# Performance work log

Hardware: AMD Instinct MI355X
Metric: run time of the kernel (lower is better)

The kernel has to match this reference:

```python
import jax, jax.numpy as jnp
import numpy as np
from jax import lax


def _gauss1d(size, sigma):
    k = np.arange(size, dtype=np.float32) - (size - 1) / 2.0
    k = np.exp(-0.5 * (k / sigma) ** 2)
    return k / k.sum()


def _make_kernel(scale, sigma):
    # make_odd
    kx, ky, kz = [s + 1 if s % 2 == 0 else s for s in scale]
    kH = _gauss1d(kx, sigma)
    kW = _gauss1d(ky, sigma)
    kD = _gauss1d(kz, sigma)
    kern = kH[:, None, None] * kW[None, :, None] * kD[None, None, :]  # (kx, ky, kz)
    kern = np.transpose(kern, (2, 0, 1))  # permute(2,0,1) -> (kz, kx, ky)
    return jnp.asarray(kern, dtype=jnp.float32)


def setup_inputs() -> dict:
    key = jax.random.key(0)
    x = jax.random.normal(key, (2, 1, 256, 256, 256), dtype=jnp.float32)
    kernel0 = _make_kernel((2, 2, 2), 1.0)  # (3,3,3)
    kernel1 = _make_kernel((4, 4, 4), 1.0)  # (5,5,5)
    return {"x": x, "kernel0": kernel0, "kernel1": kernel1}


def _blur_down(x, kernel, stride):
    # replicate pad by k//2 per spatial dim, then depthwise (C=1) conv3d.
    pad = [(0, 0), (0, 0)] + [(k // 2, k // 2) for k in kernel.shape]
    xp = jnp.pad(x, pad, mode='edge')
    # strided VALID conv == full blur followed by [::s] slicing (output ceil(H/s))
    return lax.conv_general_dilated(
        xp, kernel[None, None].astype(x.dtype),
        window_strides=stride, padding='VALID',
        dimension_numbers=('NCDHW', 'OIDHW', 'NCDHW'))


def reference(x, kernel0, kernel1):
    d1 = _blur_down(x, kernel0, (2, 2, 2))  # (2,1,128,128,128)
    d2 = _blur_down(x, kernel1, (4, 4, 4))  # (2,1,64,64,64)
    return (x, d1, d2)
```

## Files before the change

### kernel.cpp

```cpp
#include <hip/hip_runtime.h>

#define N_BATCH 2
#define S_IN 256
#define S_D1 128
#define S_D2 64
#define IN_PER_BATCH (S_IN * S_IN * S_IN)
#define D1_PER_BATCH (S_D1 * S_D1 * S_D1)
#define D2_PER_BATCH (S_D2 * S_D2 * S_D2)
#define X_ELEMS (N_BATCH * IN_PER_BATCH)
#define D1_ELEMS (N_BATCH * D1_PER_BATCH)
#define D2_ELEMS (N_BATCH * D2_PER_BATCH)

__global__ __launch_bounds__(256) void d1_kernel(
    const float* __restrict__ x, const float* __restrict__ kern,
    float* __restrict__ out)
{
    __shared__ float kw[27];
    if (threadIdx.x < 27) kw[threadIdx.x] = kern[threadIdx.x];
    __syncthreads();

    int t = blockIdx.x * blockDim.x + threadIdx.x;
    if (t >= D1_ELEMS) return;

    int w = t & (S_D1 - 1);
    int h = (t >> 7) & (S_D1 - 1);
    int d = (t >> 14) & (S_D1 - 1);
    int n = t >> 21;

    const float* xb = x + (size_t)n * IN_PER_BATCH;

    float acc = 0.0f;
#pragma unroll
    for (int a = 0; a < 3; ++a) {
        int iz = 2 * d - 1 + a;
        iz = iz < 0 ? 0 : (iz > S_IN - 1 ? S_IN - 1 : iz);
#pragma unroll
        for (int b = 0; b < 3; ++b) {
            int iy = 2 * h - 1 + b;
            iy = iy < 0 ? 0 : (iy > S_IN - 1 ? S_IN - 1 : iy);
            const float* row = xb + ((size_t)iz * S_IN + iy) * S_IN;
            const float* kr = kw + (a * 3 + b) * 3;
#pragma unroll
            for (int c = 0; c < 3; ++c) {
                int ix = 2 * w - 1 + c;
                ix = ix < 0 ? 0 : (ix > S_IN - 1 ? S_IN - 1 : ix);
                acc = fmaf(kr[c], row[ix], acc);
            }
        }
    }
    out[t] = acc;
}

__global__ __launch_bounds__(256) void d2_kernel(
    const float* __restrict__ x, const float* __restrict__ kern,
    float* __restrict__ out)
{
    __shared__ float kw[125];
    if (threadIdx.x < 125) kw[threadIdx.x] = kern[threadIdx.x];
    __syncthreads();

    int t = blockIdx.x * blockDim.x + threadIdx.x;
    if (t >= D2_ELEMS) return;

    int w = t & (S_D2 - 1);
    int h = (t >> 6) & (S_D2 - 1);
    int d = (t >> 12) & (S_D2 - 1);
    int n = t >> 18;

    const float* xb = x + (size_t)n * IN_PER_BATCH;

    float acc = 0.0f;
#pragma unroll
    for (int a = 0; a < 5; ++a) {
        int iz = 4 * d - 2 + a;
        iz = iz < 0 ? 0 : (iz > S_IN - 1 ? S_IN - 1 : iz);
#pragma unroll
        for (int b = 0; b < 5; ++b) {
            int iy = 4 * h - 2 + b;
            iy = iy < 0 ? 0 : (iy > S_IN - 1 ? S_IN - 1 : iy);
            const float* row = xb + ((size_t)iz * S_IN + iy) * S_IN;
            const float* kr = kw + (a * 5 + b) * 5;
#pragma unroll
            for (int c = 0; c < 5; ++c) {
                int ix = 4 * w - 2 + c;
                ix = ix < 0 ? 0 : (ix > S_IN - 1 ? S_IN - 1 : ix);
                acc = fmaf(kr[c], row[ix], acc);
            }
        }
    }
    out[t] = acc;
}

extern "C" void kernel_launch(void* const* d_in, const int* in_sizes, int n_in,
                              void* d_out, int out_size, void* d_ws, size_t ws_size,
                              hipStream_t stream) {
    const float* x  = (const float*)d_in[0];
    const float* k0 = (const float*)d_in[1];
    const float* k1 = (const float*)d_in[2];

    float* out0 = (float*)d_out;
    float* out1 = out0 + X_ELEMS;
    float* out2 = out1 + D1_ELEMS;

    hipMemcpyAsync(out0, x, (size_t)X_ELEMS * sizeof(float),
                   hipMemcpyDeviceToDevice, stream);

    {
        int threads = 256;
        int blocks = (D1_ELEMS + threads - 1) / threads;
        d1_kernel<<<blocks, threads, 0, stream>>>(x, k0, out1);
    }

    {
        int threads = 256;
        int blocks = (D2_ELEMS + threads - 1) / threads;
        d2_kernel<<<blocks, threads, 0, stream>>>(x, k1, out2);
    }
}
```

Baseline: 318.4 us.

## Fuse identity copy and both blur-downsample levels into one LDS-tiled kernel

Replaces the device-to-device memcpy and the two separate strided-blur kernels with a single kernel. Each block loads a haloed 12x12x72 tile of the input into shared memory using float4 loads with edge clamping. From that tile it writes the identity copy, the 3x3x3 stride-2 output and the 5x5x5 stride-4 output, reducing the latter across 4 lanes with shuffles. The goal is to read the input once instead of three times and to remove the uncoalesced global gathers. The cost is halo over-fetch of about 2.5x per tile, which relies on L2 for neighbouring tiles, plus about 41KB of LDS per block.

```diff
diff --git a/kernel.cpp b/kernel.cpp
--- a/kernel.cpp
+++ b/kernel.cpp
@@ -1,94 +1,139 @@
 #include <hip/hip_runtime.h>
 
-#define N_BATCH 2
 #define S_IN 256
 #define S_D1 128
 #define S_D2 64
 #define IN_PER_BATCH (S_IN * S_IN * S_IN)
 #define D1_PER_BATCH (S_D1 * S_D1 * S_D1)
 #define D2_PER_BATCH (S_D2 * S_D2 * S_D2)
-#define X_ELEMS (N_BATCH * IN_PER_BATCH)
-#define D1_ELEMS (N_BATCH * D1_PER_BATCH)
-#define D2_ELEMS (N_BATCH * D2_PER_BATCH)
+#define X_ELEMS (2 * IN_PER_BATCH)
+#define D1_ELEMS (2 * D1_PER_BATCH)
+#define D2_ELEMS (2 * D2_PER_BATCH)
 
-__global__ __launch_bounds__(256) void d1_kernel(
-    const float* __restrict__ x, const float* __restrict__ kern,
-    float* __restrict__ out)
+#define TD 8
+#define TH 8
+#define TW 64
+#define LZ (TD + 4)
+#define LY (TH + 4)
+#define LX (TW + 8)
+#define LDS_ELEMS (LZ * LY * LX)
+
+__global__ __launch_bounds__(256) void fused_pyramid(
+    const float* __restrict__ x, const float* __restrict__ k0,
+    const float* __restrict__ k1, float* __restrict__ out0,
+    float* __restrict__ out1, float* __restrict__ out2)
 {
-    __shared__ float kw[27];
-    if (threadIdx.x < 27) kw[threadIdx.x] = kern[threadIdx.x];
-    __syncthreads();
+    __shared__ float ls[LDS_ELEMS];
+    __shared__ float kw0[27];
+    __shared__ float kw1[125];
 
-    int t = blockIdx.x * blockDim.x + threadIdx.x;
-    if (t >= D1_ELEMS) return;
+    const int tid = threadIdx.x;
+    if (tid < 27) kw0[tid] = k0[tid];
+    else if (tid >= 32 && tid < 32 + 125) kw1[tid - 32] = k1[tid - 32];
 
-    int w = t & (S_D1 - 1);
-    int h = (t >> 7) & (S_D1 - 1);
-    int d = (t >> 14) & (S_D1 - 1);
-    int n = t >> 21;
+    const int bx = blockIdx.x;
+    const int wt = bx & 3;
+    const int hy = (bx >> 2) & 31;
+    const int dz = (bx >> 7) & 31;
+    const int n  = bx >> 12;
+
+    const int x0 = wt * TW;
+    const int y0 = hy * TH;
+    const int z0 = dz * TD;
 
     const float* xb = x + (size_t)n * IN_PER_BATCH;
 
-    float acc = 0.0f;
+    for (int v = tid; v < 144 * 18; v += 256) {
+        int row = v / 18;
+        int j   = v - row * 18;
+        int lz  = row / LY;
+        int ly  = row - lz * LY;
+        int gz = z0 + lz - 2; gz = gz < 0 ? 0 : (gz > S_IN - 1 ? S_IN - 1 : gz);
+        int gy = y0 + ly - 2; gy = gy < 0 ? 0 : (gy > S_IN - 1 ? S_IN - 1 : gy);
+        const float* rp = xb + ((size_t)gz * S_IN + gy) * S_IN;
+        int gx = x0 - 4 + 4 * j;
+        float4 val;
+        if (gx >= 0 && gx <= S_IN - 4) {
+            val = *reinterpret_cast<const float4*>(rp + gx);
+        } else {
+            float s = rp[gx < 0 ? 0 : (S_IN - 1)];
+            val = make_float4(s, s, s, s);
+        }
+        *reinterpret_cast<float4*>(&ls[(lz * LY + ly) * LX + 4 * j]) = val;
+    }
+    __syncthreads();
+
+    {
+        float* ob0 = out0 + (size_t)n * IN_PER_BATCH;
 #pragma unroll
-    for (int a = 0; a < 3; ++a) {
-        int iz = 2 * d - 1 + a;
-        iz = iz < 0 ? 0 : (iz > S_IN - 1 ? S_IN - 1 : iz);
+        for (int i = 0; i < 4; ++i) {
+            int v   = tid + 256 * i;
+            int row = v >> 4;
+            int j   = v & 15;
+            int lz  = row >> 3;
+            int ly  = row & 7;
+            float4 val = *reinterpret_cast<const float4*>(
+                &ls[((lz + 2) * LY + (ly + 2)) * LX + 4 + 4 * j]);
+            int gz = z0 + lz, gy = y0 + ly, gxo = x0 + 4 * j;
+            *reinterpret_cast<float4*>(
+                &ob0[((size_t)gz * S_IN + gy) * S_IN + gxo]) = val;
+        }
+    }
+
+    {
+        float* ob1 = out1 + (size_t)n * D1_PER_BATCH;
+        const int ox  = tid & 31;
+        const int oy  = (tid >> 5) & 3;
+        const int ozb = tid >> 7;
 #pragma unroll
-        for (int b = 0; b < 3; ++b) {
-            int iy = 2 * h - 1 + b;
-            iy = iy < 0 ? 0 : (iy > S_IN - 1 ? S_IN - 1 : iy);
-            const float* row = xb + ((size_t)iz * S_IN + iy) * S_IN;
-            const float* kr = kw + (a * 3 + b) * 3;
+        for (int it = 0; it < 2; ++it) {
+            int oz = ozb + 2 * it;
+            float acc = 0.0f;
 #pragma unroll
-            for (int c = 0; c < 3; ++c) {
-                int ix = 2 * w - 1 + c;
-                ix = ix < 0 ? 0 : (ix > S_IN - 1 ? S_IN - 1 : ix);
-                acc = fmaf(kr[c], row[ix], acc);
+            for (int a = 0; a < 3; ++a) {
+                int lz = 2 * oz + a + 1;
+#pragma unroll
+                for (int b = 0; b < 3; ++b) {
+                    int ly = 2 * oy + b + 1;
+                    const float* lr = &ls[(lz * LY + ly) * LX + 2 * ox + 3];
+                    const float* kr = &kw0[(a * 3 + b) * 3];
+                    acc = fmaf(kr[0], lr[0], acc);
+                    acc = fmaf(kr[1], lr[1], acc);
+                    acc = fmaf(kr[2], lr[2], acc);
+                }
+            }
+            int d = dz * 4 + oz, h = hy * 4 + oy, w = wt * 32 + ox;
+            ob1[((size_t)d * S_D1 + h) * S_D1 + w] = acc;
+        }
+    }
+
+    {
+        float* ob2 = out2 + (size_t)n * D2_PER_BATCH;
+        const int q  = tid & 3;
+        const int o  = tid >> 2;
+        const int ox = o & 15;
+        const int oy = (o >> 4) & 1;
+        const int oz = o >> 5;
+        float acc = 0.0f;
+        for (int a = q; a < 5; a += 4) {
+            int lz = 4 * oz + a;
+#pragma unroll
+            for (int b = 0; b < 5; ++b) {
+                int ly = 4 * oy + b;
+                const float* lr = &ls[(lz * LY + ly) * LX + 4 * ox + 2];
+                const float* kr = &kw1[(a * 5 + b) * 5];
+#pragma unroll
+                for (int c = 0; c < 5; ++c)
+                    acc = fmaf(kr[c], lr[c], acc);
             }
         }
-    }
-    out[t] = acc;
-}
-
-__global__ __launch_bounds__(256) void d2_kernel(
-    const float* __restrict__ x, const float* __restrict__ kern,
-    float* __restrict__ out)
-{
-    __shared__ float kw[125];
-    if (threadIdx.x < 125) kw[threadIdx.x] = kern[threadIdx.x];
-    __syncthreads();
-
-    int t = blockIdx.x * blockDim.x + threadIdx.x;
-    if (t >= D2_ELEMS) return;
-
-    int w = t & (S_D2 - 1);
-    int h = (t >> 6) & (S_D2 - 1);
-    int d = (t >> 12) & (S_D2 - 1);
-    int n = t >> 18;
-
-    const float* xb = x + (size_t)n * IN_PER_BATCH;
-
-    float acc = 0.0f;
-#pragma unroll
-    for (int a = 0; a < 5; ++a) {
-        int iz = 4 * d - 2 + a;
-        iz = iz < 0 ? 0 : (iz > S_IN - 1 ? S_IN - 1 : iz);
-#pragma unroll
-        for (int b = 0; b < 5; ++b) {
-            int iy = 4 * h - 2 + b;
-            iy = iy < 0 ? 0 : (iy > S_IN - 1 ? S_IN - 1 : iy);
-            const float* row = xb + ((size_t)iz * S_IN + iy) * S_IN;
-            const float* kr = kw + (a * 5 + b) * 5;
-#pragma unroll
-            for (int c = 0; c < 5; ++c) {
-                int ix = 4 * w - 2 + c;
-                ix = ix < 0 ? 0 : (ix > S_IN - 1 ? S_IN - 1 : ix);
-                acc = fmaf(kr[c], row[ix], acc);
-            }
+        acc += __shfl_xor(acc, 1);
+        acc += __shfl_xor(acc, 2);
+        if (q == 0) {
+            int d = dz * 2 + oz, h = hy * 2 + oy, w = wt * 16 + ox;
+            ob2[((size_t)d * S_D2 + h) * S_D2 + w] = acc;
         }
     }
-    out[t] = acc;
 }
 
 extern "C" void kernel_launch(void* const* d_in, const int* in_sizes, int n_in,
@@ -102,18 +147,6 @@
     float* out1 = out0 + X_ELEMS;
     float* out2 = out1 + D1_ELEMS;
 
-    hipMemcpyAsync(out0, x, (size_t)X_ELEMS * sizeof(float),
-                   hipMemcpyDeviceToDevice, stream);
-
-    {
-        int threads = 256;
-        int blocks = (D1_ELEMS + threads - 1) / threads;
-        d1_kernel<<<blocks, threads, 0, stream>>>(x, k0, out1);
-    }
-
-    {
-        int threads = 256;
-        int blocks = (D2_ELEMS + threads - 1) / threads;
-        d2_kernel<<<blocks, threads, 0, stream>>>(x, k1, out2);
-    }
+    const int blocks = 4 * 32 * 32 * 2;
+    fused_pyramid<<<blocks, 256, 0, stream>>>(x, k0, k1, out0, out1, out2);
 }
```

New measurement: 338.6 us. 6.4% more time.
